# Optimization experiments

Measured on AMD Instinct MI355X. Metric: run time of the kernel, lower is better.

## Reference

```python
import jax, jax.numpy as jnp
import numpy as np

# Each of the 16 binary logic gates, relaxed to real values, is a multilinear
# function: gate(a,b) = c0 + c1*a + c2*b + c3*a*b. Rows follow the standard
# difflogic ordering: FALSE, AND, a&~b, a, ~a&b, b, XOR, OR, NOR, XNOR,
# ~b, a|~b, ~a, ~a|b, NAND, TRUE.
GATE_COEF = jnp.array([
    [0.0,  0.0,  0.0,  0.0],   # 0:  false
    [0.0,  0.0,  0.0,  1.0],   # 1:  a AND b
    [0.0,  1.0,  0.0, -1.0],   # 2:  a AND NOT b
    [0.0,  1.0,  0.0,  0.0],   # 3:  a
    [0.0,  0.0,  1.0, -1.0],   # 4:  NOT a AND b
    [0.0,  0.0,  1.0,  0.0],   # 5:  b
    [0.0,  1.0,  1.0, -2.0],   # 6:  a XOR b
    [0.0,  1.0,  1.0, -1.0],   # 7:  a OR b
    [1.0, -1.0, -1.0,  1.0],   # 8:  NOR
    [1.0, -1.0, -1.0,  2.0],   # 9:  XNOR
    [1.0,  0.0, -1.0,  0.0],   # 10: NOT b
    [1.0,  0.0, -1.0,  1.0],   # 11: a OR NOT b
    [1.0, -1.0,  0.0,  0.0],   # 12: NOT a
    [1.0, -1.0,  0.0,  1.0],   # 13: NOT a OR b
    [1.0,  0.0,  0.0, -1.0],   # 14: NAND
    [1.0,  0.0,  0.0,  0.0],   # 15: true
], dtype=jnp.float32)

B, IN_DIM, HIDDEN, N_LAYERS, OUT_DIM, TAU = 4096, 1024, 8192, 6, 8, 10.0
NPO = HIDDEN // OUT_DIM  # neurons_per_output


def logic_layer(h, w, ia, ib):
    # h: [B, in_dim]; w: [H, 16]; ia, ib: [H] int indices into in_dim.
    # Softmax-weighted blend of 16 gates == multilinear form with blended coefs.
    p = jax.nn.softmax(w, axis=-1)          # [H, 16]
    c = p @ GATE_COEF                       # [H, 4]
    a = h[:, ia]                            # [B, H] gather
    b = h[:, ib]                            # [B, H] gather
    return c[:, 0] + c[:, 1] * a + c[:, 2] * b + c[:, 3] * (a * b)


def setup_inputs() -> dict:
    key = jax.random.key(0)
    ks = jax.random.split(key, 8)
    return {
        "x": jax.random.uniform(ks[0], (B, IN_DIM), dtype=jnp.float32),
        "logic_w": jax.random.normal(ks[1], (N_LAYERS, HIDDEN, 16), dtype=jnp.float32),
        "scaler_w": jax.random.normal(ks[2], (OUT_DIM, OUT_DIM), dtype=jnp.float32) * 0.1,
        "scaler_b": jax.random.normal(ks[3], (OUT_DIM,), dtype=jnp.float32) * 0.1,
        "idx0_a": jax.random.randint(ks[4], (HIDDEN,), 0, IN_DIM, dtype=jnp.int32),
        "idx0_b": jax.random.randint(ks[5], (HIDDEN,), 0, IN_DIM, dtype=jnp.int32),
        "idx_a": jax.random.randint(ks[6], (N_LAYERS - 1, HIDDEN), 0, HIDDEN, dtype=jnp.int32),
        "idx_b": jax.random.randint(ks[7], (N_LAYERS - 1, HIDDEN), 0, HIDDEN, dtype=jnp.int32),
    }


def reference(x, logic_w, scaler_w, scaler_b, idx0_a, idx0_b, idx_a, idx_b):
    h = (x.reshape(x.shape[0], -1) > 0.5).astype(jnp.float32)   # binarize
    h = logic_layer(h, logic_w[0], idx0_a, idx0_b)               # [B, HIDDEN]
    for i in range(N_LAYERS - 1):
        h = logic_layer(h, logic_w[i + 1], idx_a[i], idx_b[i])
    h = h.reshape(h.shape[0], OUT_DIM, NPO)                      # [B, O, NPO]
    values = jnp.sum(h, axis=2) / TAU                            # [B, O]
    q_values = values @ scaler_w.T + scaler_b                    # nn.Linear
    return q_values
```

## Files before the change

### kernel.cpp

```cpp
#include <hip/hip_runtime.h>
#include <hip/hip_fp16.h>

constexpr int BATCH    = 4096;
constexpr int IN_DIM   = 1024;
constexpr int HIDDEN   = 8192;
constexpr int N_LAYERS = 6;
constexpr int N_STAGES = N_LAYERS / 2;
constexpr int OUT_DIM  = 8;
constexpr float INV_TAU = 0.1f;

constexpr int TB   = 8;
constexpr int NTH  = 1024;
constexpr int NPT  = HIDDEN / NTH;
constexpr int NWAVES = NTH / 64;

__device__ __forceinline__ __half2 u2h(unsigned int u) {
    union { unsigned int u; __half2 h; } v; v.u = u; return v.h;
}
__device__ __forceinline__ unsigned int h2u(__half2 h) {
    union { unsigned int u; __half2 h; } v; v.h = h; return v.u;
}

__device__ __forceinline__ uint2 pack4(float4 v) {
    __half2 lo = __float22half2_rn(make_float2(v.x, v.y));
    __half2 hi = __float22half2_rn(make_float2(v.z, v.w));
    uint2 r; r.x = h2u(lo); r.y = h2u(hi); return r;
}

__device__ __forceinline__ uint2 softmax_coef(const float* __restrict__ logic_w,
                                              int l, int p) {
    const float4* w4 = (const float4*)(logic_w + ((size_t)l * HIDDEN + p) * 16);
    float4 wa = w4[0], wb = w4[1], wc = w4[2], wd = w4[3];
    float wv[16] = {wa.x, wa.y, wa.z, wa.w, wb.x, wb.y, wb.z, wb.w,
                    wc.x, wc.y, wc.z, wc.w, wd.x, wd.y, wd.z, wd.w};
    float m = wv[0];
#pragma unroll
    for (int i = 1; i < 16; ++i) m = fmaxf(m, wv[i]);
    float e[16];
    float s = 0.f;
#pragma unroll
    for (int i = 0; i < 16; ++i) { e[i] = expf(wv[i] - m); s += e[i]; }
    float inv = 1.f / s;
    const float G0[16] = {0,0,0,0,0,0,0,0, 1,1,1,1,1,1,1,1};
    const float G1[16] = {0,0,1,1,0,0,1,1, -1,-1,0,0,-1,-1,0,0};
    const float G2[16] = {0,0,0,0,1,1,1,1, -1,-1,-1,-1,0,0,0,0};
    const float G3[16] = {0,1,-1,0,-1,0,-2,-1, 1,2,0,1,0,1,-1,0};
    float c0 = 0.f, c1 = 0.f, c2 = 0.f, c3 = 0.f;
#pragma unroll
    for (int i = 0; i < 16; ++i) {
        float pv = e[i] * inv;
        c0 = fmaf(pv, G0[i], c0);
        c1 = fmaf(pv, G1[i], c1);
        c2 = fmaf(pv, G2[i], c2);
        c3 = fmaf(pv, G3[i], c3);
    }
    return pack4(make_float4(c0, c1, c2, c3));
}

__global__ void prep_kernel(const float* __restrict__ logic_w,
                            const int* __restrict__ idx0_a,
                            const int* __restrict__ idx0_b,
                            const int* __restrict__ idx_a,
                            const int* __restrict__ idx_b,
                            uint4* __restrict__ cABp,
                            uint2* __restrict__ idx4p,
                            uint2* __restrict__ cCp, int n)
{
    int id = blockIdx.x * blockDim.x + threadIdx.x;
    if (id >= n) return;
    const int s = id >> 13;
    const int j = id & (HIDDEN - 1);
    const int ltop = 2 * s + 1;
    const int lbot = 2 * s;

    const int pa = idx_a[(size_t)(ltop - 1) * HIDDEN + j];
    const int pb = idx_b[(size_t)(ltop - 1) * HIDDEN + j];

    int gaa, gba, gab, gbb;
    if (s == 0) {
        gaa = idx0_a[pa]; gba = idx0_b[pa];
        gab = idx0_a[pb]; gbb = idx0_b[pb];
    } else {
        const int* A  = idx_a + (size_t)(lbot - 1) * HIDDEN;
        const int* Bv = idx_b + (size_t)(lbot - 1) * HIDDEN;
        gaa = A[pa]; gba = Bv[pa];
        gab = A[pb]; gbb = Bv[pb];
    }
    idx4p[id] = make_uint2((unsigned)gaa | ((unsigned)gba << 16),
                           (unsigned)gab | ((unsigned)gbb << 16));

    uint2 cA = softmax_coef(logic_w, lbot, pa);
    uint2 cB = softmax_coef(logic_w, lbot, pb);
    uint2 cC = softmax_coef(logic_w, ltop, j);
    cABp[id] = make_uint4(cA.x, cA.y, cB.x, cB.y);
    cCp[id]  = cC;
}

__device__ __forceinline__ uint4 gate8(uint4 a, uint4 b, uint2 c) {
    __half2 cp01 = u2h(c.x), cp23 = u2h(c.y);
    __half2 c0 = __low2half2(cp01), c1 = __high2half2(cp01);
    __half2 c2 = __low2half2(cp23), c3 = __high2half2(cp23);
    uint4 r;
    {
        __half2 av = u2h(a.x), bv = u2h(b.x);
        r.x = h2u(__hfma2(bv, __hfma2(c3, av, c2), __hfma2(c1, av, c0)));
    }
    {
        __half2 av = u2h(a.y), bv = u2h(b.y);
        r.y = h2u(__hfma2(bv, __hfma2(c3, av, c2), __hfma2(c1, av, c0)));
    }
    {
        __half2 av = u2h(a.z), bv = u2h(b.z);
        r.z = h2u(__hfma2(bv, __hfma2(c3, av, c2), __hfma2(c1, av, c0)));
    }
    {
        __half2 av = u2h(a.w), bv = u2h(b.w);
        r.w = h2u(__hfma2(bv, __hfma2(c3, av, c2), __hfma2(c1, av, c0)));
    }
    return r;
}

__global__ __launch_bounds__(NTH) void net_kernel(
    const float*  __restrict__ x,
    const uint4*  __restrict__ cABp,
    const uint2*  __restrict__ idx4p,
    const uint2*  __restrict__ cCp,
    const float*  __restrict__ scaler_w, const float* __restrict__ scaler_b,
    float* __restrict__ out)
{
    __shared__ uint4 h[HIDDEN];
    __shared__ uint4 hx[IN_DIM];
    __shared__ float warr[NWAVES][TB];
    __shared__ float vals[TB][OUT_DIM];

    const int tid = threadIdx.x;
    const int b0  = blockIdx.x * TB;

    {
        float v[TB];
#pragma unroll
        for (int r = 0; r < TB; ++r)
            v[r] = (x[(size_t)(b0 + r) * IN_DIM + tid] > 0.5f) ? 1.f : 0.f;
        uint4 p;
        p.x = h2u(__floats2half2_rn(v[0], v[1]));
        p.y = h2u(__floats2half2_rn(v[2], v[3]));
        p.z = h2u(__floats2half2_rn(v[4], v[5]));
        p.w = h2u(__floats2half2_rn(v[6], v[7]));
        hx[tid] = p;
    }

    uint2 ij[NPT], ijn[NPT];
    uint4 acc[NPT];

#pragma unroll
    for (int k = 0; k < NPT; ++k) ij[k] = idx4p[k * NTH + tid];

    __syncthreads();

#pragma unroll
    for (int k = 0; k < NPT; ++k) ijn[k] = idx4p[HIDDEN + k * NTH + tid];
#pragma unroll
    for (int k = 0; k < NPT; ++k) {
        uint2 p = ij[k];
        uint4 x1 = hx[p.x & 0xffffu], x2 = hx[p.x >> 16];
        uint4 x3 = hx[p.y & 0xffffu], x4 = hx[p.y >> 16];
        uint4 cab = cABp[k * NTH + tid];
        uint2 cc  = cCp[k * NTH + tid];
        uint4 u = gate8(x1, x2, make_uint2(cab.x, cab.y));
        uint4 v = gate8(x3, x4, make_uint2(cab.z, cab.w));
        acc[k] = gate8(u, v, cc);
    }
#pragma unroll
    for (int k = 0; k < NPT; ++k) h[k * NTH + tid] = acc[k];
    __syncthreads();

#pragma unroll
    for (int s = 1; s < N_STAGES; ++s) {
#pragma unroll
        for (int k = 0; k < NPT; ++k) ij[k] = ijn[k];
        if (s < N_STAGES - 1) {
#pragma unroll
            for (int k = 0; k < NPT; ++k)
                ijn[k] = idx4p[(size_t)(s + 1) * HIDDEN + k * NTH + tid];
        }
#pragma unroll
        for (int k = 0; k < NPT; ++k) {
            uint2 p = ij[k];
            uint4 x1 = h[p.x & 0xffffu], x2 = h[p.x >> 16];
            uint4 x3 = h[p.y & 0xffffu], x4 = h[p.y >> 16];
            uint4 cab = cABp[(size_t)s * HIDDEN + k * NTH + tid];
            uint2 cc  = cCp[(size_t)s * HIDDEN + k * NTH + tid];
            uint4 u = gate8(x1, x2, make_uint2(cab.x, cab.y));
            uint4 v = gate8(x3, x4, make_uint2(cab.z, cab.w));
            acc[k] = gate8(u, v, cc);
        }
        __syncthreads();
#pragma unroll
        for (int k = 0; k < NPT; ++k) h[k * NTH + tid] = acc[k];
        __syncthreads();
    }

    {
        const int k    = tid >> 7;
        const int base = k * 1024 + (tid & 127);
        float s[TB] = {0.f, 0.f, 0.f, 0.f, 0.f, 0.f, 0.f, 0.f};
#pragma unroll
        for (int i = 0; i < 8; ++i) {
            uint4 t = h[base + 128 * i];
            float2 f0 = __half22float2(u2h(t.x));
            float2 f1 = __half22float2(u2h(t.y));
            float2 f2 = __half22float2(u2h(t.z));
            float2 f3 = __half22float2(u2h(t.w));
            s[0] += f0.x; s[1] += f0.y; s[2] += f1.x; s[3] += f1.y;
            s[4] += f2.x; s[5] += f2.y; s[6] += f3.x; s[7] += f3.y;
        }
#pragma unroll
        for (int off = 32; off > 0; off >>= 1) {
#pragma unroll
            for (int r = 0; r < TB; ++r) s[r] += __shfl_down(s[r], off);
        }
        if ((tid & 63) == 0) {
#pragma unroll
            for (int r = 0; r < TB; ++r) warr[tid >> 6][r] = s[r];
        }
    }
    __syncthreads();
    if (tid < TB * OUT_DIM) {
        int r = tid >> 3;
        int k = tid & 7;
        vals[r][k] = (warr[2 * k][r] + warr[2 * k + 1][r]) * INV_TAU;
    }
    __syncthreads();
    if (tid < TB * OUT_DIM) {
        int r = tid >> 3;
        int o = tid & 7;
        float q = scaler_b[o];
#pragma unroll
        for (int k = 0; k < OUT_DIM; ++k)
            q = fmaf(vals[r][k], scaler_w[o * OUT_DIM + k], q);
        out[(size_t)(b0 + r) * OUT_DIM + o] = q;
    }
}

extern "C" void kernel_launch(void* const* d_in, const int* in_sizes, int n_in,
                              void* d_out, int out_size, void* d_ws, size_t ws_size,
                              hipStream_t stream)
{
    const float* x        = (const float*)d_in[0];
    const float* logic_w  = (const float*)d_in[1];
    const float* scaler_w = (const float*)d_in[2];
    const float* scaler_b = (const float*)d_in[3];
    const int*   idx0_a   = (const int*)d_in[4];
    const int*   idx0_b   = (const int*)d_in[5];
    const int*   idx_a    = (const int*)d_in[6];
    const int*   idx_b    = (const int*)d_in[7];
    float* out = (float*)d_out;

    const int n = N_STAGES * HIDDEN;
    uint4* cABp = (uint4*)d_ws;
    uint2* idx4p = (uint2*)((char*)d_ws + (size_t)n * sizeof(uint4));
    uint2* cCp   = (uint2*)((char*)d_ws + (size_t)n * (sizeof(uint4) + sizeof(uint2)));

    prep_kernel<<<(n + 127) / 128, 128, 0, stream>>>(logic_w, idx0_a, idx0_b,
                                                     idx_a, idx_b, cABp, idx4p, cCp, n);
    net_kernel<<<BATCH / TB, NTH, 0, stream>>>(x, cABp, idx4p, cCp,
                                               scaler_w, scaler_b, out);
}
```

Baseline: 115.8 us.

## Halve batch tile to shrink LDS and dedupe softmax coefficient precompute

Cuts the per-block batch tile from 8 to 4 rows, so the packed fp16 hidden state in LDS shrinks from uint4 to uint2 per neuron. The LDS footprint per block roughly halves, which should let two 1024-thread blocks share a CU; the launch bound now also requests higher occupancy. The prep step is split in two: one kernel computes each neuron's softmax-blended coefficients once, and a second gathers them. Previously the softmax was recomputed three times per fused entry. The trade-off is twice as many blocks, each reloading the per-stage coefficient and index streams, plus a register cap that could cause spills.

```diff
diff --git a/kernel.cpp b/kernel.cpp
--- a/kernel.cpp
+++ b/kernel.cpp
@@ -9,7 +9,7 @@
 constexpr int OUT_DIM  = 8;
 constexpr float INV_TAU = 0.1f;
 
-constexpr int TB   = 8;
+constexpr int TB   = 4;
 constexpr int NTH  = 1024;
 constexpr int NPT  = HIDDEN / NTH;
 constexpr int NWAVES = NTH / 64;
@@ -27,9 +27,13 @@
     uint2 r; r.x = h2u(lo); r.y = h2u(hi); return r;
 }
 
-__device__ __forceinline__ uint2 softmax_coef(const float* __restrict__ logic_w,
-                                              int l, int p) {
-    const float4* w4 = (const float4*)(logic_w + ((size_t)l * HIDDEN + p) * 16);
+__global__ void prep_coef(const float* __restrict__ logic_w,
+                          uint2* __restrict__ coefs, int n)
+{
+    int id = blockIdx.x * blockDim.x + threadIdx.x;
+    if (id >= n) return;
+
+    const float4* w4 = (const float4*)(logic_w + (size_t)id * 16);
     float4 wa = w4[0], wb = w4[1], wc = w4[2], wd = w4[3];
     float wv[16] = {wa.x, wa.y, wa.z, wa.w, wb.x, wb.y, wb.z, wb.w,
                     wc.x, wc.y, wc.z, wc.w, wd.x, wd.y, wd.z, wd.w};
@@ -54,17 +58,17 @@
         c2 = fmaf(pv, G2[i], c2);
         c3 = fmaf(pv, G3[i], c3);
     }
-    return pack4(make_float4(c0, c1, c2, c3));
-}
-
-__global__ void prep_kernel(const float* __restrict__ logic_w,
-                            const int* __restrict__ idx0_a,
-                            const int* __restrict__ idx0_b,
-                            const int* __restrict__ idx_a,
-                            const int* __restrict__ idx_b,
-                            uint4* __restrict__ cABp,
-                            uint2* __restrict__ idx4p,
-                            uint2* __restrict__ cCp, int n)
+    coefs[id] = pack4(make_float4(c0, c1, c2, c3));
+}
+
+__global__ void prep_fuse(const uint2* __restrict__ coefs,
+                          const int* __restrict__ idx0_a,
+                          const int* __restrict__ idx0_b,
+                          const int* __restrict__ idx_a,
+                          const int* __restrict__ idx_b,
+                          uint4* __restrict__ cABp,
+                          uint2* __restrict__ idx4p,
+                          uint2* __restrict__ cCp, int n)
 {
     int id = blockIdx.x * blockDim.x + threadIdx.x;
     if (id >= n) return;
@@ -89,18 +93,17 @@
     idx4p[id] = make_uint2((unsigned)gaa | ((unsigned)gba << 16),
                            (unsigned)gab | ((unsigned)gbb << 16));
 
-    uint2 cA = softmax_coef(logic_w, lbot, pa);
-    uint2 cB = softmax_coef(logic_w, lbot, pb);
-    uint2 cC = softmax_coef(logic_w, ltop, j);
+    uint2 cA = coefs[(size_t)lbot * HIDDEN + pa];
+    uint2 cB = coefs[(size_t)lbot * HIDDEN + pb];
     cABp[id] = make_uint4(cA.x, cA.y, cB.x, cB.y);
-    cCp[id]  = cC;
-}
-
-__device__ __forceinline__ uint4 gate8(uint4 a, uint4 b, uint2 c) {
+    cCp[id]  = coefs[(size_t)ltop * HIDDEN + j];
+}
+
+__device__ __forceinline__ uint2 gate4(uint2 a, uint2 b, uint2 c) {
     __half2 cp01 = u2h(c.x), cp23 = u2h(c.y);
     __half2 c0 = __low2half2(cp01), c1 = __high2half2(cp01);
     __half2 c2 = __low2half2(cp23), c3 = __high2half2(cp23);
-    uint4 r;
+    uint2 r;
     {
         __half2 av = u2h(a.x), bv = u2h(b.x);
         r.x = h2u(__hfma2(bv, __hfma2(c3, av, c2), __hfma2(c1, av, c0)));
@@ -109,18 +112,10 @@
         __half2 av = u2h(a.y), bv = u2h(b.y);
         r.y = h2u(__hfma2(bv, __hfma2(c3, av, c2), __hfma2(c1, av, c0)));
     }
-    {
-        __half2 av = u2h(a.z), bv = u2h(b.z);
-        r.z = h2u(__hfma2(bv, __hfma2(c3, av, c2), __hfma2(c1, av, c0)));
-    }
-    {
-        __half2 av = u2h(a.w), bv = u2h(b.w);
-        r.w = h2u(__hfma2(bv, __hfma2(c3, av, c2), __hfma2(c1, av, c0)));
-    }
     return r;
 }
 
-__global__ __launch_bounds__(NTH) void net_kernel(
+__global__ __launch_bounds__(NTH, 8) void net_kernel(
     const float*  __restrict__ x,
     const uint4*  __restrict__ cABp,
     const uint2*  __restrict__ idx4p,
@@ -128,8 +123,8 @@
     const float*  __restrict__ scaler_w, const float* __restrict__ scaler_b,
     float* __restrict__ out)
 {
-    __shared__ uint4 h[HIDDEN];
-    __shared__ uint4 hx[IN_DIM];
+    __shared__ uint2 h[HIDDEN];
+    __shared__ uint2 hx[IN_DIM];
     __shared__ float warr[NWAVES][TB];
     __shared__ float vals[TB][OUT_DIM];
 
@@ -141,16 +136,14 @@
 #pragma unroll
         for (int r = 0; r < TB; ++r)
             v[r] = (x[(size_t)(b0 + r) * IN_DIM + tid] > 0.5f) ? 1.f : 0.f;
-        uint4 p;
+        uint2 p;
         p.x = h2u(__floats2half2_rn(v[0], v[1]));
         p.y = h2u(__floats2half2_rn(v[2], v[3]));
-        p.z = h2u(__floats2half2_rn(v[4], v[5]));
-        p.w = h2u(__floats2half2_rn(v[6], v[7]));
         hx[tid] = p;
     }
 
     uint2 ij[NPT], ijn[NPT];
-    uint4 acc[NPT];
+    uint2 acc[NPT];
 
 #pragma unroll
     for (int k = 0; k < NPT; ++k) ij[k] = idx4p[k * NTH + tid];
@@ -162,13 +155,13 @@
 #pragma unroll
     for (int k = 0; k < NPT; ++k) {
         uint2 p = ij[k];
-        uint4 x1 = hx[p.x & 0xffffu], x2 = hx[p.x >> 16];
-        uint4 x3 = hx[p.y & 0xffffu], x4 = hx[p.y >> 16];
+        uint2 x1 = hx[p.x & 0xffffu], x2 = hx[p.x >> 16];
+        uint2 x3 = hx[p.y & 0xffffu], x4 = hx[p.y >> 16];
         uint4 cab = cABp[k * NTH + tid];
         uint2 cc  = cCp[k * NTH + tid];
-        uint4 u = gate8(x1, x2, make_uint2(cab.x, cab.y));
-        uint4 v = gate8(x3, x4, make_uint2(cab.z, cab.w));
-        acc[k] = gate8(u, v, cc);
+        uint2 u = gate4(x1, x2, make_uint2(cab.x, cab.y));
+        uint2 v = gate4(x3, x4, make_uint2(cab.z, cab.w));
+        acc[k] = gate4(u, v, cc);
     }
 #pragma unroll
     for (int k = 0; k < NPT; ++k) h[k * NTH + tid] = acc[k];
@@ -186,13 +179,13 @@
 #pragma unroll
         for (int k = 0; k < NPT; ++k) {
             uint2 p = ij[k];
-            uint4 x1 = h[p.x & 0xffffu], x2 = h[p.x >> 16];
-            uint4 x3 = h[p.y & 0xffffu], x4 = h[p.y >> 16];
+            uint2 x1 = h[p.x & 0xffffu], x2 = h[p.x >> 16];
+            uint2 x3 = h[p.y & 0xffffu], x4 = h[p.y >> 16];
             uint4 cab = cABp[(size_t)s * HIDDEN + k * NTH + tid];
             uint2 cc  = cCp[(size_t)s * HIDDEN + k * NTH + tid];
-            uint4 u = gate8(x1, x2, make_uint2(cab.x, cab.y));
-            uint4 v = gate8(x3, x4, make_uint2(cab.z, cab.w));
-            acc[k] = gate8(u, v, cc);
+            uint2 u = gate4(x1, x2, make_uint2(cab.x, cab.y));
+            uint2 v = gate4(x3, x4, make_uint2(cab.z, cab.w));
+            acc[k] = gate4(u, v, cc);
         }
         __syncthreads();
 #pragma unroll
@@ -203,16 +196,13 @@
     {
         const int k    = tid >> 7;
         const int base = k * 1024 + (tid & 127);
-        float s[TB] = {0.f, 0.f, 0.f, 0.f, 0.f, 0.f, 0.f, 0.f};
+        float s[TB] = {0.f, 0.f, 0.f, 0.f};
 #pragma unroll
         for (int i = 0; i < 8; ++i) {
-            uint4 t = h[base + 128 * i];
+            uint2 t = h[base + 128 * i];
             float2 f0 = __half22float2(u2h(t.x));
             float2 f1 = __half22float2(u2h(t.y));
-            float2 f2 = __half22float2(u2h(t.z));
-            float2 f3 = __half22float2(u2h(t.w));
             s[0] += f0.x; s[1] += f0.y; s[2] += f1.x; s[3] += f1.y;
-            s[4] += f2.x; s[5] += f2.y; s[6] += f3.x; s[7] += f3.y;
         }
 #pragma unroll
         for (int off = 32; off > 0; off >>= 1) {
@@ -256,13 +246,17 @@
     const int*   idx_b    = (const int*)d_in[7];
     float* out = (float*)d_out;
 
-    const int n = N_STAGES * HIDDEN;
-    uint4* cABp = (uint4*)d_ws;
-    uint2* idx4p = (uint2*)((char*)d_ws + (size_t)n * sizeof(uint4));
-    uint2* cCp   = (uint2*)((char*)d_ws + (size_t)n * (sizeof(uint4) + sizeof(uint2)));
-
-    prep_kernel<<<(n + 127) / 128, 128, 0, stream>>>(logic_w, idx0_a, idx0_b,
-                                                     idx_a, idx_b, cABp, idx4p, cCp, n);
+    const int nc = N_LAYERS * HIDDEN;
+    const int nf = N_STAGES * HIDDEN;
+    char* ws = (char*)d_ws;
+    uint2* coefs = (uint2*)ws;                                   ws += (size_t)nc * sizeof(uint2);
+    uint4* cABp  = (uint4*)ws;                                   ws += (size_t)nf * sizeof(uint4);
+    uint2* idx4p = (uint2*)ws;                                   ws += (size_t)nf * sizeof(uint2);
+    uint2* cCp   = (uint2*)ws;
+
+    prep_coef<<<(nc + 255) / 256, 256, 0, stream>>>(logic_w, coefs, nc);
+    prep_fuse<<<(nf + 255) / 256, 256, 0, stream>>>(coefs, idx0_a, idx0_b,
+                                                    idx_a, idx_b, cABp, idx4p, cCp, nf);
     net_kernel<<<BATCH / TB, NTH, 0, stream>>>(x, cABp, idx4p, cCp,
                                                scaler_w, scaler_b, out);
 }
```

Measured after the change: 140.0 us. 1.21x slower.

## Split softmax coef prep into own kernel and prefetch coefficients across stages

Applied to the files above, without the earlier changes.

Softmax coefficients are now computed once per neuron in a separate kernel instead of being recomputed three times per fused entry with gathered 64-byte weight reads. The fused prep kernel then only gathers packed coefficients. In the network kernel, per-stage coefficient loads are prefetched into registers one stage ahead, like the index prefetch, to hide global latency. This adds a kernel launch and raises register pressure in a 1024-thread block, which may cause spills.

```diff
diff --git a/kernel.cpp b/kernel.cpp
--- a/kernel.cpp
+++ b/kernel.cpp
@@ -27,9 +27,13 @@
     uint2 r; r.x = h2u(lo); r.y = h2u(hi); return r;
 }
 
-__device__ __forceinline__ uint2 softmax_coef(const float* __restrict__ logic_w,
-                                              int l, int p) {
-    const float4* w4 = (const float4*)(logic_w + ((size_t)l * HIDDEN + p) * 16);
+__global__ void prep_coef(const float* __restrict__ logic_w,
+                          uint2* __restrict__ coefs, int n)
+{
+    int id = blockIdx.x * blockDim.x + threadIdx.x;
+    if (id >= n) return;
+
+    const float4* w4 = (const float4*)(logic_w + (size_t)id * 16);
     float4 wa = w4[0], wb = w4[1], wc = w4[2], wd = w4[3];
     float wv[16] = {wa.x, wa.y, wa.z, wa.w, wb.x, wb.y, wb.z, wb.w,
                     wc.x, wc.y, wc.z, wc.w, wd.x, wd.y, wd.z, wd.w};
@@ -54,17 +58,17 @@
         c2 = fmaf(pv, G2[i], c2);
         c3 = fmaf(pv, G3[i], c3);
     }
-    return pack4(make_float4(c0, c1, c2, c3));
-}
-
-__global__ void prep_kernel(const float* __restrict__ logic_w,
-                            const int* __restrict__ idx0_a,
-                            const int* __restrict__ idx0_b,
-                            const int* __restrict__ idx_a,
-                            const int* __restrict__ idx_b,
-                            uint4* __restrict__ cABp,
-                            uint2* __restrict__ idx4p,
-                            uint2* __restrict__ cCp, int n)
+    coefs[id] = pack4(make_float4(c0, c1, c2, c3));
+}
+
+__global__ void prep_fuse(const uint2* __restrict__ coefs,
+                          const int* __restrict__ idx0_a,
+                          const int* __restrict__ idx0_b,
+                          const int* __restrict__ idx_a,
+                          const int* __restrict__ idx_b,
+                          uint4* __restrict__ cABp,
+                          uint2* __restrict__ idx4p,
+                          uint2* __restrict__ cCp, int n)
 {
     int id = blockIdx.x * blockDim.x + threadIdx.x;
     if (id >= n) return;
@@ -89,11 +93,10 @@
     idx4p[id] = make_uint2((unsigned)gaa | ((unsigned)gba << 16),
                            (unsigned)gab | ((unsigned)gbb << 16));
 
-    uint2 cA = softmax_coef(logic_w, lbot, pa);
-    uint2 cB = softmax_coef(logic_w, lbot, pb);
-    uint2 cC = softmax_coef(logic_w, ltop, j);
+    uint2 cA = coefs[(size_t)lbot * HIDDEN + pa];
+    uint2 cB = coefs[(size_t)lbot * HIDDEN + pb];
     cABp[id] = make_uint4(cA.x, cA.y, cB.x, cB.y);
-    cCp[id]  = cC;
+    cCp[id]  = coefs[(size_t)ltop * HIDDEN + j];
 }
 
 __device__ __forceinline__ uint4 gate8(uint4 a, uint4 b, uint2 c) {
@@ -150,25 +153,33 @@
     }
 
     uint2 ij[NPT], ijn[NPT];
+    uint4 cab[NPT], cabn[NPT];
+    uint2 cc[NPT], ccn[NPT];
     uint4 acc[NPT];
 
 #pragma unroll
-    for (int k = 0; k < NPT; ++k) ij[k] = idx4p[k * NTH + tid];
-
-    __syncthreads();
-
-#pragma unroll
-    for (int k = 0; k < NPT; ++k) ijn[k] = idx4p[HIDDEN + k * NTH + tid];
+    for (int k = 0; k < NPT; ++k) {
+        ij[k]  = idx4p[k * NTH + tid];
+        cab[k] = cABp[k * NTH + tid];
+        cc[k]  = cCp[k * NTH + tid];
+    }
+
+    __syncthreads();
+
+#pragma unroll
+    for (int k = 0; k < NPT; ++k) {
+        ijn[k]  = idx4p[HIDDEN + k * NTH + tid];
+        cabn[k] = cABp[HIDDEN + k * NTH + tid];
+        ccn[k]  = cCp[HIDDEN + k * NTH + tid];
+    }
 #pragma unroll
     for (int k = 0; k < NPT; ++k) {
         uint2 p = ij[k];
         uint4 x1 = hx[p.x & 0xffffu], x2 = hx[p.x >> 16];
         uint4 x3 = hx[p.y & 0xffffu], x4 = hx[p.y >> 16];
-        uint4 cab = cABp[k * NTH + tid];
-        uint2 cc  = cCp[k * NTH + tid];
-        uint4 u = gate8(x1, x2, make_uint2(cab.x, cab.y));
-        uint4 v = gate8(x3, x4, make_uint2(cab.z, cab.w));
-        acc[k] = gate8(u, v, cc);
+        uint4 u = gate8(x1, x2, make_uint2(cab[k].x, cab[k].y));
+        uint4 v = gate8(x3, x4, make_uint2(cab[k].z, cab[k].w));
+        acc[k] = gate8(u, v, cc[k]);
     }
 #pragma unroll
     for (int k = 0; k < NPT; ++k) h[k * NTH + tid] = acc[k];
@@ -177,22 +188,23 @@
 #pragma unroll
     for (int s = 1; s < N_STAGES; ++s) {
 #pragma unroll
-        for (int k = 0; k < NPT; ++k) ij[k] = ijn[k];
+        for (int k = 0; k < NPT; ++k) { ij[k] = ijn[k]; cab[k] = cabn[k]; cc[k] = ccn[k]; }
         if (s < N_STAGES - 1) {
 #pragma unroll
-            for (int k = 0; k < NPT; ++k)
-                ijn[k] = idx4p[(size_t)(s + 1) * HIDDEN + k * NTH + tid];
+            for (int k = 0; k < NPT; ++k) {
+                ijn[k]  = idx4p[(size_t)(s + 1) * HIDDEN + k * NTH + tid];
+                cabn[k] = cABp[(size_t)(s + 1) * HIDDEN + k * NTH + tid];
+                ccn[k]  = cCp[(size_t)(s + 1) * HIDDEN + k * NTH + tid];
+            }
         }
 #pragma unroll
         for (int k = 0; k < NPT; ++k) {
             uint2 p = ij[k];
             uint4 x1 = h[p.x & 0xffffu], x2 = h[p.x >> 16];
             uint4 x3 = h[p.y & 0xffffu], x4 = h[p.y >> 16];
-            uint4 cab = cABp[(size_t)s * HIDDEN + k * NTH + tid];
-            uint2 cc  = cCp[(size_t)s * HIDDEN + k * NTH + tid];
-            uint4 u = gate8(x1, x2, make_uint2(cab.x, cab.y));
-            uint4 v = gate8(x3, x4, make_uint2(cab.z, cab.w));
-            acc[k] = gate8(u, v, cc);
+            uint4 u = gate8(x1, x2, make_uint2(cab[k].x, cab[k].y));
+            uint4 v = gate8(x3, x4, make_uint2(cab[k].z, cab[k].w));
+            acc[k] = gate8(u, v, cc[k]);
         }
         __syncthreads();
 #pragma unroll
@@ -256,13 +268,17 @@
     const int*   idx_b    = (const int*)d_in[7];
     float* out = (float*)d_out;
 
-    const int n = N_STAGES * HIDDEN;
-    uint4* cABp = (uint4*)d_ws;
-    uint2* idx4p = (uint2*)((char*)d_ws + (size_t)n * sizeof(uint4));
-    uint2* cCp   = (uint2*)((char*)d_ws + (size_t)n * (sizeof(uint4) + sizeof(uint2)));
-
-    prep_kernel<<<(n + 127) / 128, 128, 0, stream>>>(logic_w, idx0_a, idx0_b,
-                                                     idx_a, idx_b, cABp, idx4p, cCp, n);
+    const int nc = N_LAYERS * HIDDEN;
+    const int nf = N_STAGES * HIDDEN;
+    char* ws = (char*)d_ws;
+    uint2* coefs = (uint2*)ws;                                   ws += (size_t)nc * sizeof(uint2);
+    uint4* cABp  = (uint4*)ws;                                   ws += (size_t)nf * sizeof(uint4);
+    uint2* idx4p = (uint2*)ws;                                   ws += (size_t)nf * sizeof(uint2);
+    uint2* cCp   = (uint2*)ws;
+
+    prep_coef<<<(nc + 255) / 256, 256, 0, stream>>>(logic_w, coefs, nc);
+    prep_fuse<<<(nf + 255) / 256, 256, 0, stream>>>(coefs, idx0_a, idx0_b,
+                                                    idx_a, idx_b, cABp, idx4p, cCp, nf);
     net_kernel<<<BATCH / TB, NTH, 0, stream>>>(x, cABp, idx4p, cCp,
                                                scaler_w, scaler_b, out);
 }
```

Measured after the change: 136.5 us. 17.9% more time.
